# Performance work log

Hardware: AMD Instinct MI355X
Metric: run time of the kernel (lower is better)

Reference implementation:

```python
import jax, jax.numpy as jnp
import numpy as np

HID = 100  # LSTM hidden size (fixed in module)


def _lstm_final(x, Wih, Whh, bih, bhh, reverse):
    # x: [N, T, Hin]; returns final hidden state [N, HID] (PyTorch gate order i,f,g,o)
    xs = jnp.flip(x, axis=1) if reverse else x
    pre = jnp.einsum('nth,gh->ntg', xs, Wih) + bih + bhh  # [N, T, 4*HID]
    N = x.shape[0]
    h0 = jnp.zeros((N, HID), x.dtype)
    c0 = jnp.zeros((N, HID), x.dtype)

    def step(carry, pt):
        h, c = carry
        g = pt + h @ Whh.T
        i, f, gg, o = jnp.split(g, 4, axis=-1)
        c = jax.nn.sigmoid(f) * c + jax.nn.sigmoid(i) * jnp.tanh(gg)
        h = jax.nn.sigmoid(o) * jnp.tanh(c)
        return (h, c), None

    (h, c), _ = jax.lax.scan(step, (h0, c0), jnp.swapaxes(pre, 0, 1))
    return h


def setup_inputs():
    key = jax.random.key(0)
    ks = jax.random.split(key, 16)
    H, B, S, NP, PL = 768, 40, 128, 100, 20
    w = lambda k, shape: jax.random.normal(k, shape, jnp.float32) * 0.02
    return {
        'bert_output': jax.random.normal(ks[0], (B, S, H), jnp.float32),
        'commonsense': jax.random.normal(ks[1], (B * NP, PL, H), jnp.float32),
        'attention_mask': jnp.ones((B, S), jnp.int32),
        'commonsense_mask': jnp.ones((B, NP), jnp.int32),
        'b_size': 8, 'num_cand': 5, 'num_path': NP, 'path_len': PL,
        'lstm_Wih_f': w(ks[2], (4 * HID, H)), 'lstm_Whh_f': w(ks[3], (4 * HID, HID)),
        'lstm_bih_f': jnp.zeros((4 * HID,), jnp.float32), 'lstm_bhh_f': jnp.zeros((4 * HID,), jnp.float32),
        'lstm_Wih_b': w(ks[4], (4 * HID, H)), 'lstm_Whh_b': w(ks[5], (4 * HID, HID)),
        'lstm_bih_b': jnp.zeros((4 * HID,), jnp.float32), 'lstm_bhh_b': jnp.zeros((4 * HID,), jnp.float32),
        'proj_W': w(ks[6], (H, 2 * HID)), 'proj_b': jnp.zeros((H,), jnp.float32),
        'W1_w': w(ks[7], (1, H)), 'W1_b': jnp.zeros((1,), jnp.float32),
        'W2_w': w(ks[8], (1, H)), 'W2_b': jnp.zeros((1,), jnp.float32),
        'W3': w(ks[9], (1, 1, H)),
        'attp_W': w(ks[10], (H, 4 * H)), 'attp_b': jnp.zeros((H,), jnp.float32),
        'ln_w': jnp.ones((H,), jnp.float32), 'ln_b': jnp.zeros((H,), jnp.float32),
    }


def reference(bert_output, commonsense, attention_mask, commonsense_mask,
              b_size, num_cand, num_path, path_len,
              lstm_Wih_f, lstm_Whh_f, lstm_bih_f, lstm_bhh_f,
              lstm_Wih_b, lstm_Whh_b, lstm_bih_b, lstm_bhh_b,
              proj_W, proj_b, W1_w, W1_b, W2_w, W2_b, W3,
              attp_W, attp_b, ln_w, ln_b):
    Bc = b_size * num_cand
    # bidirectional LSTM over commonsense paths; only final hidden states are used
    h_f = _lstm_final(commonsense, lstm_Wih_f, lstm_Whh_f, lstm_bih_f, lstm_bhh_f, False)
    h_b = _lstm_final(commonsense, lstm_Wih_b, lstm_Whh_b, lstm_bih_b, lstm_bhh_b, True)
    enc = jnp.concatenate([h_f, h_b], axis=-1)               # [Bc*NP, 200]
    cs = jax.nn.relu(enc @ proj_W.T + proj_b).reshape(Bc, num_path, -1)  # [B, P, H]
    # trilinear BiDAF-style scores
    part1 = bert_output @ W1_w.T + W1_b                      # [B, S, 1]
    part2 = (cs @ W2_w.T + W2_b).transpose(0, 2, 1)          # [B, 1, P]
    part3 = jnp.einsum('bsh,bph->bsp', W3 * bert_output, cs)  # [B, S, P]
    mask_cs = (1.0 - commonsense_mask.astype(jnp.float32)) * -10000.0
    mask_dqa = (1.0 - attention_mask.astype(jnp.float32)) * -10000.0
    total = part1 + part2 + part3 + mask_cs[:, None, :] + mask_dqa[:, :, None]
    cs_att = jax.nn.softmax(total, axis=-1)                  # over paths
    weight_cs = jnp.einsum('bsp,bph->bsh', cs_att, cs)
    ctx_att = jax.nn.softmax(total, axis=1)                  # over context tokens
    probs = jnp.einsum('bsp,btp->bst', cs_att, ctx_att)      # [B, S, S]
    weighted_context = jnp.einsum('bst,bth->bsh', probs, bert_output)
    cat = jnp.concatenate([bert_output, weight_cs, bert_output * weight_cs,
                           bert_output * weighted_context], axis=-1)
    x = jax.nn.relu(cat @ attp_W.T + attp_b) + bert_output
    u = x.mean(-1, keepdims=True)
    s = ((x - u) ** 2).mean(-1, keepdims=True)
    return ln_w * ((x - u) / jnp.sqrt(s + 1e-12)) + ln_b
```

## Files before the change

### kernel.cpp

```cpp
#include <hip/hip_runtime.h>


typedef unsigned short ushort_t;
typedef unsigned int u32;
typedef __attribute__((ext_vector_type(8))) short short8;
typedef __attribute__((ext_vector_type(4))) float f32x4;
typedef __attribute__((address_space(1))) const u32 gu32;
typedef __attribute__((address_space(3))) u32 lu32;

__device__ __forceinline__ ushort_t f2bf(float f) {
  u32 x = __builtin_bit_cast(u32, f);
  u32 r = (x + 0x7fffu + ((x >> 16) & 1u)) >> 16;
  return (ushort_t)r;
}
__device__ __forceinline__ float bflo(u32 u) { return __builtin_bit_cast(float, u << 16); }
__device__ __forceinline__ float bfhi(u32 u) { return __builtin_bit_cast(float, u & 0xffff0000u); }
__device__ __forceinline__ u32 cvtpk(float lo, float hi) {
  u32 r;
  asm("v_cvt_pk_bf16_f32 %0, %1, %2" : "=v"(r) : "v"(lo), "v"(hi));
  return r;
}

__device__ __forceinline__ float sigm(float x) { return 1.f / (1.f + __expf(-x)); }
__device__ __forceinline__ float tanh_f(float x) { return 1.f - 2.f / (__expf(2.f * x) + 1.f); }


__global__ __launch_bounds__(256) void prep_all(
    const float* __restrict__ Wih_f, const float* __restrict__ Wih_b,
    const float* __restrict__ Whh_f, const float* __restrict__ Whh_b,
    const float* __restrict__ bih_f, const float* __restrict__ bhh_f,
    const float* __restrict__ bih_b, const float* __restrict__ bhh_b,
    const float* __restrict__ projW, const float* __restrict__ attpW,
    ushort_t* __restrict__ wihcat, ushort_t* __restrict__ whhcat,
    float* __restrict__ biascat, ushort_t* __restrict__ projw_bf,
    ushort_t* __restrict__ attpw_bf,
    const float* __restrict__ bert, const float* __restrict__ W3,
    ushort_t* __restrict__ bw3, ushort_t* __restrict__ bT, ushort_t* __restrict__ cat,
    const float4* __restrict__ x4, ushort_t* __restrict__ xb,
    const float* __restrict__ W1w, const float* __restrict__ W1b,
    float* __restrict__ part1)
{
  __shared__ ushort_t tl[64 * 130];
  int bid = blockIdx.x, tid = threadIdx.x;
  if (bid < 512) {
    const int TOT = 614400 + 102400 + 800 + 196608 + 2359296;
    for (int idx = bid * 256 + tid; idx < TOT; idx += 512 * 256) {
      if (idx < 614400) {
        int g = idx / 768, k = idx % 768;
        float v = g < 400 ? Wih_f[g * 768 + k] : Wih_b[(g - 400) * 768 + k];
        wihcat[idx] = f2bf(v);
      } else if (idx < 716800) {
        int e = idx - 614400; int g = e / 128, j = e % 128;
        float v = 0.f;
        if (j < 100) v = g < 400 ? Whh_f[g * 100 + j] : Whh_b[(g - 400) * 100 + j];
        whhcat[e] = f2bf(v);
      } else if (idx < 717600) {
        int g = idx - 716800;
        biascat[g] = g < 400 ? bih_f[g] + bhh_f[g] : bih_b[g - 400] + bhh_b[g - 400];
      } else if (idx < 914208) {
        int e = idx - 717600; int o = e / 256, j = e % 256;
        float v = 0.f;
        if (j < 100) v = projW[o * 200 + j];
        else if (j >= 128 && j < 228) v = projW[o * 200 + 100 + (j - 128)];
        projw_bf[e] = f2bf(v);
      } else {
        int e = idx - 914208;
        attpw_bf[e] = f2bf(attpW[e]);
      }
    }
  } else if (bid < 992) {
    int e0 = bid - 512;
    int ht = e0 % 12, b = e0 / 12;
    int h0 = ht * 64;
    for (int e = tid; e < 8192; e += 256) {
      int t = e >> 6, hh = e & 63;
      float v = bert[((size_t)b * 128 + t) * 768 + h0 + hh];
      ushort_t vb = f2bf(v);
      bw3[((size_t)b * 128 + t) * 768 + h0 + hh] = f2bf(v * W3[h0 + hh]);
      cat[((size_t)b * 128 + t) * 3072 + h0 + hh] = vb;
      tl[hh * 130 + t] = vb;
    }
    __syncthreads();
    for (int e = tid; e < 8192; e += 256) {
      int hh = e >> 7, t = e & 127;
      bT[((size_t)b * 768 + h0 + hh) * 128 + t] = tl[hh * 130 + t];
    }
  } else if (bid < 3040) {
    for (int i = (bid - 992) * 256 + tid; i < 15360000; i += 2048 * 256) {
      int seq = i / 3840;
      int rem = i - seq * 3840;
      int t = rem / 192;
      int k4 = rem - t * 192;
      float4 v = x4[i];
      ushort4 o;
      o.x = f2bf(v.x); o.y = f2bf(v.y); o.z = f2bf(v.z); o.w = f2bf(v.w);
      *reinterpret_cast<ushort4*>(&xb[((size_t)t * 4000 + seq) * 768 + k4 * 4]) = o;
    }
  } else {
    int row = (bid - 3040) * 4 + (tid >> 6);
    int lane = tid & 63;
    const float* x = bert + (size_t)row * 768;
    float s = 0.f;
    for (int k = lane; k < 768; k += 64) s += x[k] * W1w[k];
    for (int off = 32; off; off >>= 1) s += __shfl_down(s, off);
    if (lane == 0) part1[row] = s + W1b[0];
  }
}


__global__ __launch_bounds__(256) void gemm_pre160(
    const ushort_t* __restrict__ A,
    const ushort_t* __restrict__ B,
    const float* __restrict__ bias,
    ushort_t* __restrict__ P)
{
  __shared__ __align__(16) ushort_t lsA[2][128 * 64];
  __shared__ __align__(16) ushort_t lsB[2][160 * 64];
  int bid = blockIdx.x;
  int xcd = bid & 7, slot = bid >> 3;
  int L = (xcd < 5) ? xcd * 391 + slot : 1955 + (xcd - 5) * 390 + slot;
  int bm = L / 5, bn = L - bm * 5;
  int m0 = bm * 128, n0 = bn * 160;
  int tid = threadIdx.x, lane = tid & 63, w = tid >> 6;
  int wr = w >> 1, wc = w & 1;
  int l15 = lane & 15, lk = lane >> 4;
  f32x4 acc[4][5];
  #pragma unroll
  for (int i = 0; i < 4; ++i)
    #pragma unroll
    for (int j = 0; j < 5; ++j)
      #pragma unroll
      for (int r = 0; r < 4; ++r) acc[i][j][r] = 0.f;

  int r_in = lane >> 3, p = lane & 7;
  auto stage = [&](int kt, int bf) {
    #pragma unroll
    for (int i = 0; i < 4; ++i) {
      int seg = w * 4 + i;
      int row = seg * 8 + r_in;
      int sl = p ^ (row & 7);
      __builtin_amdgcn_global_load_lds(
          (gu32*)(A + (size_t)(m0 + row) * 768 + kt * 64 + sl * 8),
          (lu32*)(&lsA[bf][seg * 512]), 16, 0, 0);
    }
    #pragma unroll
    for (int i = 0; i < 5; ++i) {
      int seg = w * 5 + i;
      int row = seg * 8 + r_in;
      int sl = p ^ (row & 7);
      __builtin_amdgcn_global_load_lds(
          (gu32*)(B + (size_t)(n0 + row) * 768 + kt * 64 + sl * 8),
          (lu32*)(&lsB[bf][seg * 512]), 16, 0, 0);
    }
  };

  stage(0, 0);
  #pragma unroll 1
  for (int kt = 0; kt < 12; ++kt) {
    int bf = kt & 1;
    if (kt < 11) {
      stage(kt + 1, bf ^ 1);
      asm volatile("s_waitcnt vmcnt(9)" ::: "memory");
    } else {
      asm volatile("s_waitcnt vmcnt(0)" ::: "memory");
    }
    __builtin_amdgcn_s_barrier();
    __builtin_amdgcn_sched_barrier(0);
    #pragma unroll
    for (int ks = 0; ks < 2; ++ks) {
      short8 af[4], bfv[5];
      #pragma unroll
      for (int f = 0; f < 4; ++f) {
        int row = wr * 64 + f * 16 + l15;
        af[f] = *reinterpret_cast<const short8*>(
            &lsA[bf][row * 64 + (((ks * 4 + lk) ^ (row & 7)) << 3)]);
      }
      #pragma unroll
      for (int f = 0; f < 5; ++f) {
        int rowb = wc * 80 + f * 16 + l15;
        bfv[f] = *reinterpret_cast<const short8*>(
            &lsB[bf][rowb * 64 + (((ks * 4 + lk) ^ (rowb & 7)) << 3)]);
      }
      #pragma unroll
      for (int fm = 0; fm < 4; ++fm)
        #pragma unroll
        for (int fn = 0; fn < 5; ++fn)
          acc[fm][fn] = __builtin_amdgcn_mfma_f32_16x16x32_bf16(af[fm], bfv[fn], acc[fm][fn], 0, 0, 0);
    }
    __builtin_amdgcn_s_barrier();
  }
  #pragma unroll
  for (int fm = 0; fm < 4; ++fm) {
    int mb = m0 + wr * 64 + fm * 16;
    int t = mb / 4000;
    int sq = mb - t * 4000;
    int cch = sq >> 4;
    #pragma unroll
    for (int fn = 0; fn < 5; ++fn) {
      int nb = n0 + wc * 80 + fn * 16;
      int nl = nb < 400 ? nb : nb - 400;
      int nq = (nb < 400 ? 0 : 25) + (nl >> 4);
      float bsv = bias[nb + l15];
      uint2 pk;
      pk.x = cvtpk(acc[fm][fn][0] + bsv, acc[fm][fn][1] + bsv);
      pk.y = cvtpk(acc[fm][fn][2] + bsv, acc[fm][fn][3] + bsv);
      *reinterpret_cast<uint2*>(
          &P[((((size_t)t * 250 + cch) * 50 + nq) << 8) + l15 * 16 + lk * 4]) = pk;
    }
  }
}


__global__ __launch_bounds__(256) void gemm_proj(
    const ushort_t* __restrict__ A, int lda,
    const ushort_t* __restrict__ B, int ldb,
    int M, int N, int KT,
    const float* __restrict__ bias,
    float* __restrict__ C, int ldc,
    ushort_t* __restrict__ C2,
    ushort_t* __restrict__ csT)
{
  __shared__ __align__(16) ushort_t lsA[128 * 64];
  __shared__ __align__(16) ushort_t lsB[128 * 64];
  int bm = blockIdx.x, bn = blockIdx.y;
  int m0 = bm * 128, n0 = bn * 128;
  int tid = threadIdx.x, lane = tid & 63, w = tid >> 6;
  int wr = w >> 1, wc = w & 1;
  int l15 = lane & 15, lk = lane >> 4;
  f32x4 acc[4][4];
  #pragma unroll
  for (int i = 0; i < 4; ++i)
    #pragma unroll
    for (int j = 0; j < 4; ++j)
      #pragma unroll
      for (int r = 0; r < 4; ++r) acc[i][j][r] = 0.f;

  int r_in = lane >> 3, p = lane & 7;
  for (int kt = 0; kt < KT; ++kt) {
    __syncthreads();
    #pragma unroll
    for (int i = 0; i < 4; ++i) {
      int seg = w * 4 + i;
      int row = seg * 8 + r_in;
      int sl = p ^ (row & 7);
      int m = m0 + row;
      if (m < M)
        __builtin_amdgcn_global_load_lds(
            (gu32*)(A + (size_t)m * lda + kt * 64 + sl * 8),
            (lu32*)(lsA + seg * 512), 16, 0, 0);
      int n = n0 + row;
      if (n < N)
        __builtin_amdgcn_global_load_lds(
            (gu32*)(B + (size_t)n * ldb + kt * 64 + sl * 8),
            (lu32*)(lsB + seg * 512), 16, 0, 0);
    }
    __syncthreads();
    #pragma unroll
    for (int ks = 0; ks < 2; ++ks) {
      short8 af[4], bfv[4];
      #pragma unroll
      for (int f = 0; f < 4; ++f) {
        int row = wr * 64 + f * 16 + l15;
        af[f] = *reinterpret_cast<const short8*>(
            &lsA[row * 64 + (((ks * 4 + lk) ^ (row & 7)) << 3)]);
        int rowb = wc * 64 + f * 16 + l15;
        bfv[f] = *reinterpret_cast<const short8*>(
            &lsB[rowb * 64 + (((ks * 4 + lk) ^ (rowb & 7)) << 3)]);
      }
      #pragma unroll
      for (int fm = 0; fm < 4; ++fm)
        #pragma unroll
        for (int fn = 0; fn < 4; ++fn)
          acc[fm][fn] = __builtin_amdgcn_mfma_f32_16x16x32_bf16(af[fm], bfv[fn], acc[fm][fn], 0, 0, 0);
    }
  }
  #pragma unroll
  for (int fm = 0; fm < 4; ++fm)
    #pragma unroll
    for (int fn = 0; fn < 4; ++fn)
      #pragma unroll
      for (int r = 0; r < 4; ++r) {
        int m = m0 + wr * 64 + fm * 16 + lk * 4 + r;
        int n = n0 + wc * 64 + fn * 16 + l15;
        if (m < M && n < N) {
          float v = fmaxf(acc[fm][fn][r] + bias[n], 0.f);
          C[(size_t)m * ldc + n] = v;
          ushort_t vb = f2bf(v);
          C2[(size_t)m * ldc + n] = vb;
          int bq = m / 100, pq = m - bq * 100;
          csT[((size_t)bq * 896 + n) * 128 + pq] = vb;
        }
      }
}


template <int EPI>
__global__ __launch_bounds__(256) void gemm128b(
    const ushort_t* __restrict__ A, long long sA, int lda,
    const ushort_t* __restrict__ Bm, long long sB, int ldb,
    int M, int N, int KT,
    float* __restrict__ Cf, ushort_t* __restrict__ Cb,
    const float* __restrict__ bertp, ushort_t* __restrict__ catp)
{
  __shared__ __align__(16) ushort_t lsA[128 * 64];
  __shared__ __align__(16) ushort_t lsB[128 * 64];
  int b = blockIdx.z;
  int koff = blockIdx.y * KT * 64;
  const ushort_t* Ab = A + (size_t)b * sA;
  const ushort_t* Bb = Bm + (size_t)b * sB;
  int n0 = blockIdx.x * 128;
  int tid = threadIdx.x, lane = tid & 63, w = tid >> 6;
  int wr = w >> 1, wc = w & 1;
  int l15 = lane & 15, lk = lane >> 4;
  f32x4 acc[4][4];
  #pragma unroll
  for (int i = 0; i < 4; ++i)
    #pragma unroll
    for (int j = 0; j < 4; ++j)
      #pragma unroll
      for (int r = 0; r < 4; ++r) acc[i][j][r] = 0.f;

  int r_in = lane >> 3, p = lane & 7;
  for (int kt = 0; kt < KT; ++kt) {
    __syncthreads();
    #pragma unroll
    for (int i = 0; i < 4; ++i) {
      int seg = w * 4 + i;
      int row = seg * 8 + r_in;
      int sl = p ^ (row & 7);
      if (row < M)
        __builtin_amdgcn_global_load_lds(
            (gu32*)(Ab + (size_t)row * lda + koff + kt * 64 + sl * 8),
            (lu32*)(lsA + seg * 512), 16, 0, 0);
      int n = n0 + row;
      if (n < N)
        __builtin_amdgcn_global_load_lds(
            (gu32*)(Bb + (size_t)n * ldb + koff + kt * 64 + sl * 8),
            (lu32*)(lsB + seg * 512), 16, 0, 0);
    }
    __syncthreads();
    #pragma unroll
    for (int ks = 0; ks < 2; ++ks) {
      short8 af[4], bfv[4];
      #pragma unroll
      for (int f = 0; f < 4; ++f) {
        int row = wr * 64 + f * 16 + l15;
        af[f] = *reinterpret_cast<const short8*>(
            &lsA[row * 64 + (((ks * 4 + lk) ^ (row & 7)) << 3)]);
        int rowb = wc * 64 + f * 16 + l15;
        bfv[f] = *reinterpret_cast<const short8*>(
            &lsB[rowb * 64 + (((ks * 4 + lk) ^ (rowb & 7)) << 3)]);
      }
      #pragma unroll
      for (int fm = 0; fm < 4; ++fm)
        #pragma unroll
        for (int fn = 0; fn < 4; ++fn)
          acc[fm][fn] = __builtin_amdgcn_mfma_f32_16x16x32_bf16(af[fm], bfv[fn], acc[fm][fn], 0, 0, 0);
    }
  }
  #pragma unroll
  for (int fm = 0; fm < 4; ++fm)
    #pragma unroll
    for (int fn = 0; fn < 4; ++fn)
      #pragma unroll
      for (int r = 0; r < 4; ++r) {
        int m = wr * 64 + fm * 16 + lk * 4 + r;
        int n = n0 + wc * 64 + fn * 16 + l15;
        if (m < M && n < N) {
          float v = acc[fm][fn][r];
          if (EPI == 10) {
            Cf[(size_t)blockIdx.y * 512000 + (size_t)b * 12800 + (size_t)m * 100 + n] = v;
          } else if (EPI == 12) {
            size_t row3 = ((size_t)b * 128 + m) * 3072;
            if (n < 768) {
              float bv = bertp[((size_t)b * 128 + m) * 768 + n];
              ushort_t wv = f2bf(v);
              catp[row3 + 768 + n] = wv;
              catp[row3 + 1536 + n] = f2bf(bv * bflo((u32)wv));
            } else {
              Cb[(size_t)b * 16384 + (size_t)m * 128 + (n - 768)] = f2bf(v);
            }
          } else {
            float bv = bertp[((size_t)b * 128 + m) * 768 + n];
            catp[((size_t)b * 128 + m) * 3072 + 2304 + n] = f2bf(bv * v);
          }
        }
      }
}


__global__ __launch_bounds__(256) void gemm64_attp(
    const ushort_t* __restrict__ A,
    const ushort_t* __restrict__ B,
    const float* __restrict__ bias,
    const float* __restrict__ resid,
    float* __restrict__ C)
{
  __shared__ __align__(16) ushort_t lsA[2][64 * 64];
  __shared__ __align__(16) ushort_t lsB[2][128 * 64];
  int bid = blockIdx.x;
  int xcd = bid & 7, slot = bid >> 3;
  int L = xcd * 60 + slot;
  int bm = L / 6, bn = L - bm * 6;
  int m0 = bm * 64, n0 = bn * 128;
  int tid = threadIdx.x, lane = tid & 63, w = tid >> 6;
  int wr = w >> 1, wc = w & 1;
  int l15 = lane & 15, lk = lane >> 4;
  f32x4 acc[2][4];
  #pragma unroll
  for (int i = 0; i < 2; ++i)
    #pragma unroll
    for (int j = 0; j < 4; ++j)
      #pragma unroll
      for (int r = 0; r < 4; ++r) acc[i][j][r] = 0.f;

  int r_in = lane >> 3, p = lane & 7;
  auto stage = [&](int kt, int bf) {
    #pragma unroll
    for (int i = 0; i < 2; ++i) {
      int seg = w * 2 + i;
      int row = seg * 8 + r_in;
      int sl = p ^ (row & 7);
      __builtin_amdgcn_global_load_lds(
          (gu32*)(A + (size_t)(m0 + row) * 3072 + kt * 64 + sl * 8),
          (lu32*)(&lsA[bf][seg * 512]), 16, 0, 0);
    }
    #pragma unroll
    for (int i = 0; i < 4; ++i) {
      int seg = w * 4 + i;
      int row = seg * 8 + r_in;
      int sl = p ^ (row & 7);
      __builtin_amdgcn_global_load_lds(
          (gu32*)(B + (size_t)(n0 + row) * 3072 + kt * 64 + sl * 8),
          (lu32*)(&lsB[bf][seg * 512]), 16, 0, 0);
    }
  };

  stage(0, 0);
  #pragma unroll 1
  for (int kt = 0; kt < 48; ++kt) {
    int bf = kt & 1;
    if (kt < 47) {
      stage(kt + 1, bf ^ 1);
      asm volatile("s_waitcnt vmcnt(6)" ::: "memory");
    } else {
      asm volatile("s_waitcnt vmcnt(0)" ::: "memory");
    }
    __builtin_amdgcn_s_barrier();
    __builtin_amdgcn_sched_barrier(0);
    #pragma unroll
    for (int ks = 0; ks < 2; ++ks) {
      short8 af[2], bfv[4];
      #pragma unroll
      for (int f = 0; f < 2; ++f) {
        int row = wr * 32 + f * 16 + l15;
        af[f] = *reinterpret_cast<const short8*>(
            &lsA[bf][row * 64 + (((ks * 4 + lk) ^ (row & 7)) << 3)]);
      }
      #pragma unroll
      for (int f = 0; f < 4; ++f) {
        int rowb = wc * 64 + f * 16 + l15;
        bfv[f] = *reinterpret_cast<const short8*>(
            &lsB[bf][rowb * 64 + (((ks * 4 + lk) ^ (rowb & 7)) << 3)]);
      }
      #pragma unroll
      for (int fm = 0; fm < 2; ++fm)
        #pragma unroll
        for (int fn = 0; fn < 4; ++fn)
          acc[fm][fn] = __builtin_amdgcn_mfma_f32_16x16x32_bf16(af[fm], bfv[fn], acc[fm][fn], 0, 0, 0);
    }
    __builtin_amdgcn_s_barrier();
  }
  #pragma unroll
  for (int fm = 0; fm < 2; ++fm)
    #pragma unroll
    for (int fn = 0; fn < 4; ++fn)
      #pragma unroll
      for (int r = 0; r < 4; ++r) {
        int m = m0 + wr * 32 + fm * 16 + lk * 4 + r;
        int n = n0 + wc * 64 + fn * 16 + l15;
        float v = fmaxf(acc[fm][fn][r] + bias[n], 0.f) + resid[(size_t)m * 768 + n];
        C[(size_t)m * 768 + n] = v;
      }
}


__global__ __launch_bounds__(256) void lstm_recur(
    const ushort_t* __restrict__ pre,
    const ushort_t* __restrict__ whh,
    ushort_t* __restrict__ hcat)
{
  __shared__ __align__(16) ushort_t gx[25 * 256];
  __shared__ __align__(16) ushort_t h_lds[16 * 128];

  int dir = blockIdx.y;
  int c = blockIdx.x;
  int tid = threadIdx.x, lane = tid & 63, w = tid >> 6;
  int s = lane & 15, lk = lane >> 4;

  short8 wf[7][4];
  #pragma unroll
  for (int qi = 0; qi < 7; ++qi) {
    int q = w + qi * 4;
    if (q < 25) {
      const ushort_t* wp = whh + ((size_t)dir * 400 + q * 16 + s) * 128;
      #pragma unroll
      for (int ks = 0; ks < 4; ++ks)
        wf[qi][ks] = *reinterpret_cast<const short8*>(wp + ks * 32 + lk * 8);
    }
  }
  for (int e = tid; e < 1024; e += 256)
    *reinterpret_cast<u32*>(&h_lds[e * 2]) = 0u;

  float cst[2][4];
  #pragma unroll
  for (int g = 0; g < 2; ++g)
    #pragma unroll
    for (int r = 0; r < 4; ++r) cst[g][r] = 0.f;

  uint2 pvA[7], pvB[7];
  {
    int tt0 = dir ? 19 : 0;
    const ushort_t* pb = pre + ((((size_t)tt0 * 250 + c) * 50 + dir * 25) << 8);
    #pragma unroll
    for (int qi = 0; qi < 7; ++qi) {
      int q = w + qi * 4;
      if (q < 25) pvA[qi] = *reinterpret_cast<const uint2*>(pb + (q << 8) + s * 16 + lk * 4);
    }
  }
  __syncthreads();

  auto step = [&](uint2 (&pvc)[7], uint2 (&pvn)[7], int t) {
    f32x4 acc[7];
    #pragma unroll
    for (int qi = 0; qi < 7; ++qi)
      #pragma unroll
      for (int r = 0; r < 4; ++r) acc[qi][r] = 0.f;
    #pragma unroll
    for (int ks = 0; ks < 4; ++ks) {
      short8 af = *reinterpret_cast<const short8*>(
          &h_lds[s * 128 + (((ks * 4 + lk) ^ s) << 3)]);
      #pragma unroll
      for (int qi = 0; qi < 7; ++qi)
        if (w + qi * 4 < 25)
          acc[qi] = __builtin_amdgcn_mfma_f32_16x16x32_bf16(af, wf[qi][ks], acc[qi], 0, 0, 0);
    }
    #pragma unroll
    for (int qi = 0; qi < 7; ++qi)
      if (w + qi * 4 < 25) {
        acc[qi][0] += bflo(pvc[qi].x); acc[qi][1] += bfhi(pvc[qi].x);
        acc[qi][2] += bflo(pvc[qi].y); acc[qi][3] += bfhi(pvc[qi].y);
      }
    if (t + 1 < 20) {
      int tn = dir ? 19 - (t + 1) : (t + 1);
      const ushort_t* pb = pre + ((((size_t)tn * 250 + c) * 50 + dir * 25) << 8);
      #pragma unroll
      for (int qi = 0; qi < 7; ++qi) {
        int q = w + qi * 4;
        if (q < 25) pvn[qi] = *reinterpret_cast<const uint2*>(pb + (q << 8) + s * 16 + lk * 4);
      }
    }
    #pragma unroll
    for (int qi = 0; qi < 7; ++qi) {
      int q = w + qi * 4;
      if (q < 25) {
        ushort4 pk;
        pk.x = f2bf(acc[qi][0]); pk.y = f2bf(acc[qi][1]);
        pk.z = f2bf(acc[qi][2]); pk.w = f2bf(acc[qi][3]);
        *reinterpret_cast<ushort4*>(&gx[(q << 8) + s * 16 + lk * 4]) = pk;
      }
    }
    __syncthreads();
    #pragma unroll
    for (int gd = 0; gd < 2; ++gd) {
      int gi = w + gd * 4;
      if (gi < 7) {
        int j = gi * 16 + s;
        if (j < 100) {
          auto ld2 = [&](int q, int sp) {
            return *reinterpret_cast<const uint2*>(&gx[(q << 8) + sp * 16 + lk * 4]);
          };
          uint2 iv = ld2(gi, s);
          uint2 fv = (s < 12) ? ld2(6 + gi, s + 4) : ld2(7 + gi, s - 12);
          uint2 gv = (s < 8) ? ld2(12 + gi, s + 8) : ld2(13 + gi, s - 8);
          uint2 ov = (s < 4) ? ld2(18 + gi, s + 12) : ld2(19 + gi, s - 4);
          float ia[4] = {bflo(iv.x), bfhi(iv.x), bflo(iv.y), bfhi(iv.y)};
          float fa[4] = {bflo(fv.x), bfhi(fv.x), bflo(fv.y), bfhi(fv.y)};
          float ga[4] = {bflo(gv.x), bfhi(gv.x), bflo(gv.y), bfhi(gv.y)};
          float oa[4] = {bflo(ov.x), bfhi(ov.x), bflo(ov.y), bfhi(ov.y)};
          #pragma unroll
          for (int r = 0; r < 4; ++r) {
            float cc = sigm(fa[r]) * cst[gd][r] + sigm(ia[r]) * tanh_f(ga[r]);
            cst[gd][r] = cc;
            int row = lk * 4 + r;
            h_lds[row * 128 + (((j >> 3) ^ row) << 3) + (j & 7)] =
                f2bf(sigm(oa[r]) * tanh_f(cc));
          }
        }
      }
    }
    __syncthreads();
  };

  #pragma unroll 1
  for (int tp = 0; tp < 10; ++tp) {
    step(pvA, pvB, 2 * tp);
    step(pvB, pvA, 2 * tp + 1);
  }

  {
    int row = tid >> 4, sl = tid & 15;
    uint2 v = *reinterpret_cast<const uint2*>(&h_lds[row * 128 + ((sl ^ row) << 3)]);
    *reinterpret_cast<uint2*>(&hcat[(size_t)(c * 16 + row) * 256 + dir * 128 + sl * 8]) = v;
  }
}


__global__ void rowdot_cs(const float* __restrict__ cs,
                          const float* __restrict__ W2w, const float* __restrict__ W2b,
                          float* __restrict__ part2) {
  int row = blockIdx.x * 4 + (threadIdx.x >> 6);
  int lane = threadIdx.x & 63;
  const float* x = cs + (size_t)row * 768;
  float s = 0.f;
  for (int k = lane; k < 768; k += 64) s += x[k] * W2w[k];
  for (int off = 32; off; off >>= 1) s += __shfl_down(s, off);
  if (lane == 0) part2[row] = s + W2b[0];
}

__global__ void softmax_both(const float* __restrict__ t4,
                             const float* __restrict__ part1,
                             const float* __restrict__ part2,
                             const int* __restrict__ amask,
                             const int* __restrict__ cmask,
                             ushort_t* __restrict__ csatt,
                             ushort_t* __restrict__ csTcat) {
  int bid = blockIdx.x;
  int lane = threadIdx.x;
  auto tsum = [&](size_t idx) {
    return t4[idx] + t4[idx + 512000] + t4[idx + 1024000] + t4[idx + 1536000];
  };
  if (bid < 5120) {
    int b = bid >> 7;
    size_t base = (size_t)bid * 100;
    float e0 = tsum(base + lane) + part2[b * 100 + lane]
               + (1.f - (float)cmask[b * 100 + lane]) * -10000.f;
    bool has1 = (lane + 64) < 100;
    float e1 = -3.4e38f;
    if (has1)
      e1 = tsum(base + lane + 64) + part2[b * 100 + lane + 64]
           + (1.f - (float)cmask[b * 100 + lane + 64]) * -10000.f;
    float m = fmaxf(e0, e1);
    for (int off = 32; off; off >>= 1) m = fmaxf(m, __shfl_xor(m, off));
    float s0 = expf(e0 - m), s1 = has1 ? expf(e1 - m) : 0.f;
    float s = s0 + s1;
    for (int off = 32; off; off >>= 1) s += __shfl_xor(s, off);
    float inv = 1.f / s;
    csatt[(size_t)bid * 128 + lane] = f2bf(s0 * inv);
    csatt[(size_t)bid * 128 + lane + 64] = has1 ? f2bf(s1 * inv) : (ushort_t)0;
  } else {
    int idx = bid - 5120;
    int b = idx / 100, p = idx - b * 100;
    size_t base = (size_t)b * 12800 + p;
    int t0 = lane, t1 = lane + 64;
    float e0 = tsum(base + (size_t)t0 * 100) + part1[b * 128 + t0]
               + (1.f - (float)amask[b * 128 + t0]) * -10000.f;
    float e1 = tsum(base + (size_t)t1 * 100) + part1[b * 128 + t1]
               + (1.f - (float)amask[b * 128 + t1]) * -10000.f;
    float m = fmaxf(e0, e1);
    for (int off = 32; off; off >>= 1) m = fmaxf(m, __shfl_xor(m, off));
    float s0 = expf(e0 - m), s1 = expf(e1 - m);
    float s = s0 + s1;
    for (int off = 32; off; off >>= 1) s += __shfl_xor(s, off);
    float inv = 1.f / s;
    csTcat[((size_t)b * 896 + 768 + t0) * 128 + p] = f2bf(s0 * inv);
    csTcat[((size_t)b * 896 + 768 + t1) * 128 + p] = f2bf(s1 * inv);
  }
}

__global__ __launch_bounds__(256) void layernorm(float* __restrict__ X,
                                                 const float* __restrict__ w,
                                                 const float* __restrict__ bta) {
  int row = blockIdx.x;
  float* x = X + (size_t)row * 768;
  int t = threadIdx.x;
  float v[3];
  float s = 0.f;
  #pragma unroll
  for (int i = 0; i < 3; ++i) { v[i] = x[t + 256 * i]; s += v[i]; }
  __shared__ float red[256];
  red[t] = s; __syncthreads();
  for (int off = 128; off; off >>= 1) { if (t < off) red[t] += red[t + off]; __syncthreads(); }
  float mean = red[0] * (1.f / 768.f);
  __syncthreads();
  float q = 0.f;
  #pragma unroll
  for (int i = 0; i < 3; ++i) { float d = v[i] - mean; q += d * d; }
  red[t] = q; __syncthreads();
  for (int off = 128; off; off >>= 1) { if (t < off) red[t] += red[t + off]; __syncthreads(); }
  float inv = rsqrtf(red[0] * (1.f / 768.f) + 1e-12f);
  #pragma unroll
  for (int i = 0; i < 3; ++i) {
    int k = t + 256 * i;
    x[k] = w[k] * ((v[i] - mean) * inv) + bta[k];
  }
}


extern "C" void kernel_launch(void* const* d_in, const int* in_sizes, int n_in,
                              void* d_out, int out_size, void* d_ws, size_t ws_size,
                              hipStream_t stream) {
  (void)in_sizes; (void)n_in; (void)out_size; (void)ws_size;
  const float* bert  = (const float*)d_in[0];
  const float* cmn   = (const float*)d_in[1];
  const int*   amask = (const int*)d_in[2];
  const int*   cmask = (const int*)d_in[3];
  const float* Wih_f = (const float*)d_in[8];
  const float* Whh_f = (const float*)d_in[9];
  const float* bih_f = (const float*)d_in[10];
  const float* bhh_f = (const float*)d_in[11];
  const float* Wih_b = (const float*)d_in[12];
  const float* Whh_b = (const float*)d_in[13];
  const float* bih_b = (const float*)d_in[14];
  const float* bhh_b = (const float*)d_in[15];
  const float* projW = (const float*)d_in[16];
  const float* projb = (const float*)d_in[17];
  const float* W1w   = (const float*)d_in[18];
  const float* W1b   = (const float*)d_in[19];
  const float* W2w   = (const float*)d_in[20];
  const float* W2b   = (const float*)d_in[21];
  const float* W3    = (const float*)d_in[22];
  const float* attpW = (const float*)d_in[23];
  const float* attpb = (const float*)d_in[24];
  const float* lnw   = (const float*)d_in[25];
  const float* lnb   = (const float*)d_in[26];

  char* base = (char*)d_ws;
  size_t off = 0;
  auto alloc = [&](size_t bytes) -> char* {
    char* r = base + off;
    off += (bytes + 255) & ~(size_t)255;
    return r;
  };
  ushort_t* wihcat   = (ushort_t*)alloc(800 * 768 * 2);
  ushort_t* whhcat   = (ushort_t*)alloc(800 * 128 * 2);
  float*    biascat  = (float*)alloc(800 * 4);
  ushort_t* projw_bf = (ushort_t*)alloc(768 * 256 * 2);
  ushort_t* attpw_bf = (ushort_t*)alloc(768 * 3072 * 2);
  ushort_t* hcat     = (ushort_t*)alloc(4000 * 256 * 2);
  float*    cs       = (float*)alloc((size_t)4000 * 768 * 4);
  ushort_t* cs_bf    = (ushort_t*)alloc((size_t)4000 * 768 * 2);
  ushort_t* csTcat   = (ushort_t*)alloc((size_t)40 * 896 * 128 * 2);
  float*    part1    = (float*)alloc(5120 * 4);
  float*    part2    = (float*)alloc(4000 * 4);
  float*    total4   = (float*)alloc((size_t)4 * 40 * 128 * 100 * 4);
  ushort_t* csatt_bf = (ushort_t*)alloc((size_t)40 * 128 * 128 * 2);
  ushort_t* probs_bf = (ushort_t*)alloc((size_t)40 * 128 * 128 * 2);
  ushort_t* bw3_bf   = (ushort_t*)alloc((size_t)40 * 128 * 768 * 2);
  ushort_t* bertT    = (ushort_t*)alloc((size_t)40 * 768 * 128 * 2);
  ushort_t* cat      = (ushort_t*)alloc((size_t)5120 * 3072 * 2);
  ushort_t* x_bf     = (ushort_t*)alloc((size_t)20 * 4000 * 768 * 2);
  ushort_t* pre      = (ushort_t*)alloc((size_t)20 * 250 * 50 * 256 * 2);

  prep_all<<<4320, 256, 0, stream>>>(
      Wih_f, Wih_b, Whh_f, Whh_b, bih_f, bhh_f, bih_b, bhh_b, projW, attpW,
      wihcat, whhcat, biascat, projw_bf, attpw_bf,
      bert, W3, bw3_bf, bertT, cat,
      (const float4*)cmn, x_bf,
      W1w, W1b, part1);

  gemm_pre160<<<3125, 256, 0, stream>>>(x_bf, wihcat, biascat, pre);
  lstm_recur<<<dim3(250, 2), 256, 0, stream>>>(pre, whhcat, hcat);

  gemm_proj<<<dim3(32, 6), 256, 0, stream>>>(hcat, 256, projw_bf, 256, 4000, 768, 4,
                                             projb, cs, 768, cs_bf, csTcat);
  rowdot_cs<<<1000, 256, 0, stream>>>(cs, W2w, W2b, part2);

  gemm128b<10><<<dim3(1, 4, 40), 256, 0, stream>>>(
      bw3_bf, 98304LL, 768, cs_bf, 76800LL, 768, 128, 100, 3,
      total4, nullptr, nullptr, nullptr);
  softmax_both<<<9120, 64, 0, stream>>>(total4, part1, part2, amask, cmask,
                                        csatt_bf, csTcat);
  gemm128b<12><<<dim3(7, 1, 40), 256, 0, stream>>>(
      csatt_bf, 16384LL, 128, csTcat, 114688LL, 128, 128, 896, 2,
      nullptr, probs_bf, bert, cat);
  gemm128b<13><<<dim3(6, 1, 40), 256, 0, stream>>>(
      probs_bf, 16384LL, 128, bertT, 98304LL, 128, 128, 768, 2,
      nullptr, nullptr, bert, cat);

  gemm64_attp<<<480, 256, 0, stream>>>(cat, attpw_bf, attpb, bert, (float*)d_out);
  layernorm<<<5120, 256, 0, stream>>>((float*)d_out, lnw, lnb);
}
```

Before: 481.1 us.

## Fuse trilinear score GEMM with both softmaxes in one per-batch kernel

Replaces the split-K score GEMM plus separate dual-softmax kernel with a single kernel per batch that computes the full 128x100 score tile in LDS, adds the bias and mask terms, and performs the row and column softmaxes in place. This removes the fp32 partial-sum buffer round trip through global memory and one launch. In exchange it runs only 40 blocks without split-K, and the softmax phase is serial per thread with strided column writes.

```diff
diff --git a/kernel.cpp b/kernel.cpp
--- a/kernel.cpp
+++ b/kernel.cpp
@@ -294,18 +294,124 @@
 }
 
 
+__global__ __launch_bounds__(256) void total_softmax(
+    const ushort_t* __restrict__ bw3,
+    const ushort_t* __restrict__ csb,
+    const float* __restrict__ part1,
+    const float* __restrict__ part2,
+    const int* __restrict__ amask,
+    const int* __restrict__ cmask,
+    ushort_t* __restrict__ csatt,
+    ushort_t* __restrict__ csTcat)
+{
+  __shared__ __align__(16) ushort_t lsA[128 * 64];
+  __shared__ __align__(16) ushort_t lsB[128 * 64];
+  __shared__ float tot[128 * 104];
+  int b = blockIdx.x;
+  const ushort_t* Ab = bw3 + (size_t)b * 98304;
+  const ushort_t* Bb = csb + (size_t)b * 76800;
+  int tid = threadIdx.x, lane = tid & 63, w = tid >> 6;
+  int wr = w >> 1, wc = w & 1;
+  int l15 = lane & 15, lk = lane >> 4;
+  f32x4 acc[4][4];
+  #pragma unroll
+  for (int i = 0; i < 4; ++i)
+    #pragma unroll
+    for (int j = 0; j < 4; ++j)
+      #pragma unroll
+      for (int r = 0; r < 4; ++r) acc[i][j][r] = 0.f;
+
+  for (int e = tid; e < 896; e += 256)
+    *reinterpret_cast<u32*>(&lsB[100 * 64 + e * 2]) = 0u;
+
+  int r_in = lane >> 3, p = lane & 7;
+  for (int kt = 0; kt < 12; ++kt) {
+    __syncthreads();
+    #pragma unroll
+    for (int i = 0; i < 4; ++i) {
+      int seg = w * 4 + i;
+      int row = seg * 8 + r_in;
+      int sl = p ^ (row & 7);
+      __builtin_amdgcn_global_load_lds(
+          (gu32*)(Ab + (size_t)row * 768 + kt * 64 + sl * 8),
+          (lu32*)(lsA + seg * 512), 16, 0, 0);
+      if (row < 100)
+        __builtin_amdgcn_global_load_lds(
+            (gu32*)(Bb + (size_t)row * 768 + kt * 64 + sl * 8),
+            (lu32*)(lsB + seg * 512), 16, 0, 0);
+    }
+    __syncthreads();
+    #pragma unroll
+    for (int ks = 0; ks < 2; ++ks) {
+      short8 af[4], bfv[4];
+      #pragma unroll
+      for (int f = 0; f < 4; ++f) {
+        int row = wr * 64 + f * 16 + l15;
+        af[f] = *reinterpret_cast<const short8*>(
+            &lsA[row * 64 + (((ks * 4 + lk) ^ (row & 7)) << 3)]);
+        int rowb = wc * 64 + f * 16 + l15;
+        bfv[f] = *reinterpret_cast<const short8*>(
+            &lsB[rowb * 64 + (((ks * 4 + lk) ^ (rowb & 7)) << 3)]);
+      }
+      #pragma unroll
+      for (int fm = 0; fm < 4; ++fm)
+        #pragma unroll
+        for (int fn = 0; fn < 4; ++fn)
+          acc[fm][fn] = __builtin_amdgcn_mfma_f32_16x16x32_bf16(af[fm], bfv[fn], acc[fm][fn], 0, 0, 0);
+    }
+  }
+  __syncthreads();
+  #pragma unroll
+  for (int fm = 0; fm < 4; ++fm)
+    #pragma unroll
+    for (int fn = 0; fn < 4; ++fn)
+      #pragma unroll
+      for (int r = 0; r < 4; ++r) {
+        int m = wr * 64 + fm * 16 + lk * 4 + r;
+        int n = wc * 64 + fn * 16 + l15;
+        if (n < 100) {
+          float v = acc[fm][fn][r]
+                    + part1[b * 128 + m] + (1.f - (float)amask[b * 128 + m]) * -10000.f
+                    + part2[b * 100 + n] + (1.f - (float)cmask[b * 100 + n]) * -10000.f;
+          tot[m * 104 + n] = v;
+        }
+      }
+  __syncthreads();
+  if (tid < 128) {
+    const float* row = &tot[tid * 104];
+    float mx = -3.4e38f;
+    for (int n = 0; n < 100; ++n) mx = fmaxf(mx, row[n]);
+    float s = 0.f;
+    for (int n = 0; n < 100; ++n) s += expf(row[n] - mx);
+    float inv = 1.f / s;
+    ushort_t* o = &csatt[((size_t)b * 128 + tid) * 128];
+    for (int n = 0; n < 100; ++n) o[n] = f2bf(expf(row[n] - mx) * inv);
+    for (int n = 100; n < 128; ++n) o[n] = 0;
+  }
+  if (tid >= 128 && tid < 228) {
+    int p2 = tid - 128;
+    float mx = -3.4e38f;
+    for (int m = 0; m < 128; ++m) mx = fmaxf(mx, tot[m * 104 + p2]);
+    float s = 0.f;
+    for (int m = 0; m < 128; ++m) s += expf(tot[m * 104 + p2] - mx);
+    float inv = 1.f / s;
+    for (int m = 0; m < 128; ++m)
+      csTcat[((size_t)b * 896 + 768 + m) * 128 + p2] = f2bf(expf(tot[m * 104 + p2] - mx) * inv);
+  }
+}
+
+
 template <int EPI>
 __global__ __launch_bounds__(256) void gemm128b(
     const ushort_t* __restrict__ A, long long sA, int lda,
     const ushort_t* __restrict__ Bm, long long sB, int ldb,
     int M, int N, int KT,
-    float* __restrict__ Cf, ushort_t* __restrict__ Cb,
+    ushort_t* __restrict__ Cb,
     const float* __restrict__ bertp, ushort_t* __restrict__ catp)
 {
   __shared__ __align__(16) ushort_t lsA[128 * 64];
   __shared__ __align__(16) ushort_t lsB[128 * 64];
   int b = blockIdx.z;
-  int koff = blockIdx.y * KT * 64;
   const ushort_t* Ab = A + (size_t)b * sA;
   const ushort_t* Bb = Bm + (size_t)b * sB;
   int n0 = blockIdx.x * 128;
@@ -330,12 +436,12 @@
       int sl = p ^ (row & 7);
       if (row < M)
         __builtin_amdgcn_global_load_lds(
-            (gu32*)(Ab + (size_t)row * lda + koff + kt * 64 + sl * 8),
+            (gu32*)(Ab + (size_t)row * lda + kt * 64 + sl * 8),
             (lu32*)(lsA + seg * 512), 16, 0, 0);
       int n = n0 + row;
       if (n < N)
         __builtin_amdgcn_global_load_lds(
-            (gu32*)(Bb + (size_t)n * ldb + koff + kt * 64 + sl * 8),
+            (gu32*)(Bb + (size_t)n * ldb + kt * 64 + sl * 8),
             (lu32*)(lsB + seg * 512), 16, 0, 0);
     }
     __syncthreads();
@@ -368,9 +474,7 @@
         int n = n0 + wc * 64 + fn * 16 + l15;
         if (m < M && n < N) {
           float v = acc[fm][fn][r];
-          if (EPI == 10) {
-            Cf[(size_t)blockIdx.y * 512000 + (size_t)b * 12800 + (size_t)m * 100 + n] = v;
-          } else if (EPI == 12) {
+          if (EPI == 12) {
             size_t row3 = ((size_t)b * 128 + m) * 3072;
             if (n < 768) {
               float bv = bertp[((size_t)b * 128 + m) * 768 + n];
@@ -626,56 +730,6 @@
   for (int k = lane; k < 768; k += 64) s += x[k] * W2w[k];
   for (int off = 32; off; off >>= 1) s += __shfl_down(s, off);
   if (lane == 0) part2[row] = s + W2b[0];
-}
-
-__global__ void softmax_both(const float* __restrict__ t4,
-                             const float* __restrict__ part1,
-                             const float* __restrict__ part2,
-                             const int* __restrict__ amask,
-                             const int* __restrict__ cmask,
-                             ushort_t* __restrict__ csatt,
-                             ushort_t* __restrict__ csTcat) {
-  int bid = blockIdx.x;
-  int lane = threadIdx.x;
-  auto tsum = [&](size_t idx) {
-    return t4[idx] + t4[idx + 512000] + t4[idx + 1024000] + t4[idx + 1536000];
-  };
-  if (bid < 5120) {
-    int b = bid >> 7;
-    size_t base = (size_t)bid * 100;
-    float e0 = tsum(base + lane) + part2[b * 100 + lane]
-               + (1.f - (float)cmask[b * 100 + lane]) * -10000.f;
-    bool has1 = (lane + 64) < 100;
-    float e1 = -3.4e38f;
-    if (has1)
-      e1 = tsum(base + lane + 64) + part2[b * 100 + lane + 64]
-           + (1.f - (float)cmask[b * 100 + lane + 64]) * -10000.f;
-    float m = fmaxf(e0, e1);
-    for (int off = 32; off; off >>= 1) m = fmaxf(m, __shfl_xor(m, off));
-    float s0 = expf(e0 - m), s1 = has1 ? expf(e1 - m) : 0.f;
-    float s = s0 + s1;
-    for (int off = 32; off; off >>= 1) s += __shfl_xor(s, off);
-    float inv = 1.f / s;
-    csatt[(size_t)bid * 128 + lane] = f2bf(s0 * inv);
-    csatt[(size_t)bid * 128 + lane + 64] = has1 ? f2bf(s1 * inv) : (ushort_t)0;
-  } else {
-    int idx = bid - 5120;
-    int b = idx / 100, p = idx - b * 100;
-    size_t base = (size_t)b * 12800 + p;
-    int t0 = lane, t1 = lane + 64;
-    float e0 = tsum(base + (size_t)t0 * 100) + part1[b * 128 + t0]
-               + (1.f - (float)amask[b * 128 + t0]) * -10000.f;
-    float e1 = tsum(base + (size_t)t1 * 100) + part1[b * 128 + t1]
-               + (1.f - (float)amask[b * 128 + t1]) * -10000.f;
-    float m = fmaxf(e0, e1);
-    for (int off = 32; off; off >>= 1) m = fmaxf(m, __shfl_xor(m, off));
-    float s0 = expf(e0 - m), s1 = expf(e1 - m);
-    float s = s0 + s1;
-    for (int off = 32; off; off >>= 1) s += __shfl_xor(s, off);
-    float inv = 1.f / s;
-    csTcat[((size_t)b * 896 + 768 + t0) * 128 + p] = f2bf(s0 * inv);
-    csTcat[((size_t)b * 896 + 768 + t1) * 128 + p] = f2bf(s1 * inv);
-  }
 }
 
 __global__ __launch_bounds__(256) void layernorm(float* __restrict__ X,
@@ -753,7 +807,6 @@
   ushort_t* csTcat   = (ushort_t*)alloc((size_t)40 * 896 * 128 * 2);
   float*    part1    = (float*)alloc(5120 * 4);
   float*    part2    = (float*)alloc(4000 * 4);
-  float*    total4   = (float*)alloc((size_t)4 * 40 * 128 * 100 * 4);
   ushort_t* csatt_bf = (ushort_t*)alloc((size_t)40 * 128 * 128 * 2);
   ushort_t* probs_bf = (ushort_t*)alloc((size_t)40 * 128 * 128 * 2);
   ushort_t* bw3_bf   = (ushort_t*)alloc((size_t)40 * 128 * 768 * 2);
@@ -776,17 +829,14 @@
                                              projb, cs, 768, cs_bf, csTcat);
   rowdot_cs<<<1000, 256, 0, stream>>>(cs, W2w, W2b, part2);
 
-  gemm128b<10><<<dim3(1, 4, 40), 256, 0, stream>>>(
-      bw3_bf, 98304LL, 768, cs_bf, 76800LL, 768, 128, 100, 3,
-      total4, nullptr, nullptr, nullptr);
-  softmax_both<<<9120, 64, 0, stream>>>(total4, part1, part2, amask, cmask,
+  total_softmax<<<40, 256, 0, stream>>>(bw3_bf, cs_bf, part1, part2, amask, cmask,
                                         csatt_bf, csTcat);
   gemm128b<12><<<dim3(7, 1, 40), 256, 0, stream>>>(
       csatt_bf, 16384LL, 128, csTcat, 114688LL, 128, 128, 896, 2,
-      nullptr, probs_bf, bert, cat);
+      probs_bf, bert, cat);
   gemm128b<13><<<dim3(6, 1, 40), 256, 0, stream>>>(
       probs_bf, 16384LL, 128, bertT, 98304LL, 128, 128, 768, 2,
-      nullptr, nullptr, bert, cat);
+      nullptr, bert, cat);
 
   gemm64_attp<<<480, 256, 0, stream>>>(cat, attpw_bf, attpb, bert, (float*)d_out);
   layernorm<<<5120, 256, 0, stream>>>((float*)d_out, lnw, lnb);
```

Result: no change. 482.0 us (+0.2%).
